# Kernel optimization log

Hardware: AMD Instinct MI355X
Metric: run time of the kernel (lower is better)

## Reference

```python
import jax, jax.numpy as jnp
import numpy as np

D_MODEL = 1024
N_HEAD = 16
HEAD_DIM = D_MODEL // N_HEAD
B, S = 4, 2048


def setup_inputs() -> dict:
    key = jax.random.key(0)
    ks = jax.random.split(key, 11)
    scale = 1.0 / np.sqrt(D_MODEL)
    inp = {
        "q": jax.random.normal(ks[0], (B, S, D_MODEL), jnp.float32),
        "k": jax.random.normal(ks[1], (B, S, D_MODEL), jnp.float32),
        "v": jax.random.normal(ks[2], (B, S, D_MODEL), jnp.float32),
        # torch nn.Linear weights: [out_features, in_features], y = x @ W.T + b
        "Wq": jax.random.normal(ks[3], (D_MODEL, D_MODEL), jnp.float32) * scale,
        "bq": jax.random.normal(ks[4], (D_MODEL,), jnp.float32) * scale,
        "Wk": jax.random.normal(ks[5], (D_MODEL, D_MODEL), jnp.float32) * scale,
        "bk": jax.random.normal(ks[6], (D_MODEL,), jnp.float32) * scale,
        "Wv": jax.random.normal(ks[7], (D_MODEL, D_MODEL), jnp.float32) * scale,
        "bv": jax.random.normal(ks[8], (D_MODEL,), jnp.float32) * scale,
        "Wo": jax.random.normal(ks[9], (D_MODEL, D_MODEL), jnp.float32) * scale,
        "bo": jax.random.normal(ks[10], (D_MODEL,), jnp.float32) * scale,
    }
    return inp


def _split_heads(x):
    # [B, S, D] -> [B, H, S, hd]
    b, s, _ = x.shape
    return x.reshape(b, s, N_HEAD, HEAD_DIM).transpose(0, 2, 1, 3)


def reference(q, k, v, Wq, bq, Wk, bk, Wv, bv, Wo, bo):
    qh = _split_heads(q @ Wq.T + bq)
    kh = _split_heads(k @ Wk.T + bk)
    vh = _split_heads(v @ Wv.T + bv)
    scores = jnp.einsum("bhqd,bhkd->bhqk", qh, kh) / jnp.sqrt(
        jnp.asarray(HEAD_DIM, qh.dtype)
    )
    weights = jax.nn.softmax(scores, axis=-1)  # [B, H, Sq, Sk]
    ctx = jnp.einsum("bhqk,bhkd->bhqd", weights, vh)
    b, h, s, d = ctx.shape
    ctx = ctx.transpose(0, 2, 1, 3).reshape(b, s, h * d)  # [B, S, D]
    return ctx @ Wo.T + bo
```

## Files before the change

### kernel.cpp

```cpp
#include <hip/hip_runtime.h>
#include <hip/hip_bf16.h>

typedef float   f32x4   __attribute__((ext_vector_type(4)));
typedef __bf16  bf16x8  __attribute__((ext_vector_type(8)));
typedef unsigned short u16x8 __attribute__((ext_vector_type(8)));
typedef unsigned short u16x4 __attribute__((ext_vector_type(4)));

#define DEVI __device__ __forceinline__

DEVI unsigned short f2bf_bits(float f) {
    __bf16 h = (__bf16)f;
    return __builtin_bit_cast(unsigned short, h);
}

DEVI f32x4 mfma_bf16(bf16x8 a, bf16x8 b, f32x4 c) {
    return __builtin_amdgcn_mfma_f32_16x16x32_bf16(a, b, c, 0, 0, 0);
}

template <bool A_F32, bool OUT_F32>
__global__ __launch_bounds__(256) void gemm_bt_kernel(
    const void* __restrict__ Ap, const float* __restrict__ W,
    const float* __restrict__ bias, void* __restrict__ Cp,
    int M, int N, int K, float scale)
{
    __shared__ __align__(16) char ldsA[128 * 128];
    __shared__ __align__(16) char ldsB[128 * 128];
    const int t = threadIdx.x;
    const int wave = t >> 6, lane = t & 63;
    const int g = lane >> 4, c = lane & 15;
    const int rowbase = blockIdx.x * 128;
    const int colbase = blockIdx.y * 128;
    const int wr = (wave >> 1) * 64, wc = (wave & 1) * 64;

    f32x4 acc[4][4] = {};

    for (int kt = 0; kt < K; kt += 64) {
#pragma unroll
        for (int ch = 0; ch < 4; ++ch) {
            int id = ch * 256 + t;
            int row = id >> 3;
            int col = (id & 7) * 8;
            int dst = row * 128 + ((col * 2) ^ ((row & 7) << 4));
            u16x8 hv;
            if constexpr (A_F32) {
                const float* src = (const float*)Ap + (size_t)(rowbase + row) * K + kt + col;
                f32x4 x0 = *(const f32x4*)src;
                f32x4 x1 = *(const f32x4*)(src + 4);
#pragma unroll
                for (int j = 0; j < 4; ++j) { hv[j] = f2bf_bits(x0[j]); hv[4 + j] = f2bf_bits(x1[j]); }
            } else {
                const unsigned short* src = (const unsigned short*)Ap + (size_t)(rowbase + row) * K + kt + col;
                hv = *(const u16x8*)src;
            }
            *(u16x8*)(ldsA + dst) = hv;

            const float* srcb = W + (size_t)(colbase + row) * K + kt + col;
            f32x4 y0 = *(const f32x4*)srcb;
            f32x4 y1 = *(const f32x4*)(srcb + 4);
            u16x8 hb;
#pragma unroll
            for (int j = 0; j < 4; ++j) { hb[j] = f2bf_bits(y0[j]); hb[4 + j] = f2bf_bits(y1[j]); }
            *(u16x8*)(ldsB + dst) = hb;
        }
        __syncthreads();

#pragma unroll
        for (int kk = 0; kk < 2; ++kk) {
            bf16x8 af[4], bfr[4];
#pragma unroll
            for (int i = 0; i < 4; ++i) {
                int ra = wr + i * 16 + c;
                af[i] = *(const bf16x8*)(ldsA + ra * 128 + ((kk * 64 + g * 16) ^ ((ra & 7) << 4)));
                int rb = wc + i * 16 + c;
                bfr[i] = *(const bf16x8*)(ldsB + rb * 128 + ((kk * 64 + g * 16) ^ ((rb & 7) << 4)));
            }
#pragma unroll
            for (int i = 0; i < 4; ++i)
#pragma unroll
                for (int j = 0; j < 4; ++j)
                    acc[i][j] = mfma_bf16(af[i], bfr[j], acc[i][j]);
        }
        __syncthreads();
    }

#pragma unroll
    for (int j = 0; j < 4; ++j) {
        int coln = colbase + wc + j * 16 + c;
        float bv = bias[coln];
#pragma unroll
        for (int i = 0; i < 4; ++i) {
            int row0 = rowbase + wr + i * 16 + g * 4;
#pragma unroll
            for (int r = 0; r < 4; ++r) {
                float val = (acc[i][j][r] + bv) * scale;
                if constexpr (OUT_F32)
                    ((float*)Cp)[(size_t)(row0 + r) * N + coln] = val;
                else
                    ((unsigned short*)Cp)[(size_t)(row0 + r) * N + coln] = f2bf_bits(val);
            }
        }
    }
}

__global__ __launch_bounds__(256) void transpose_v_kernel(
    const unsigned short* __restrict__ Vp, unsigned short* __restrict__ Vt)
{
    __shared__ unsigned short tile[64][72];
    const int t = threadIdx.x;
    const int bh = blockIdx.y, b = bh >> 4, h = bh & 15;
    const int s0 = blockIdx.x * 64;
#pragma unroll
    for (int ch = 0; ch < 2; ++ch) {
        int id = ch * 256 + t;
        int srow = id >> 3, dcol = (id & 7) * 8;
        u16x8 v = *(const u16x8*)(Vp + (size_t)(b * 2048 + s0 + srow) * 1024 + h * 64 + dcol);
        *(u16x8*)&tile[srow][dcol] = v;
    }
    __syncthreads();
#pragma unroll
    for (int ch = 0; ch < 2; ++ch) {
        int id = ch * 256 + t;
        int drow = id >> 3, scol = (id & 7) * 8;
        u16x8 ov;
#pragma unroll
        for (int j = 0; j < 8; ++j) ov[j] = tile[scol + j][drow];
        *(u16x8*)(Vt + (size_t)(bh * 64 + drow) * 2048 + s0 + scol) = ov;
    }
}

__global__ __launch_bounds__(256) void attn_kernel(
    const unsigned short* __restrict__ Qp, const unsigned short* __restrict__ Kp,
    const unsigned short* __restrict__ Vt, unsigned short* __restrict__ ctx)
{
    __shared__ __align__(16) char ldsK[64 * 128];
    __shared__ __align__(16) char ldsV[64 * 128];
    __shared__ __align__(16) char ldsP[4][16 * 128];
    const int t = threadIdx.x;
    const int wave = t >> 6, lane = t & 63;
    const int g = lane >> 4, c = lane & 15;
    const int bh = blockIdx.y, b = bh >> 4, h = bh & 15;
    const int qb = blockIdx.x * 64;

    bf16x8 qf[2];
    {
        const unsigned short* qrow = Qp + (size_t)(b * 2048 + qb + wave * 16 + c) * 1024 + h * 64;
        qf[0] = *(const bf16x8*)(qrow + 8 * g);
        qf[1] = *(const bf16x8*)(qrow + 32 + 8 * g);
    }

    f32x4 o[4] = {};
    float psum = 0.f;

    const int row0 = t >> 3, colB = (t & 7) * 8;
    const int row1 = 32 + row0;
    const int dst0 = row0 * 128 + ((colB * 2) ^ ((row0 & 7) << 4));
    const int dst1 = row1 * 128 + ((colB * 2) ^ ((row1 & 7) << 4));
    const unsigned short* Ksrc = Kp + (size_t)(b * 2048) * 1024 + h * 64;
    const unsigned short* Vsrc = Vt + (size_t)(bh * 64) * 2048;

    u16x8 kv0 = *(const u16x8*)(Ksrc + (size_t)row0 * 1024 + colB);
    u16x8 kv1 = *(const u16x8*)(Ksrc + (size_t)row1 * 1024 + colB);
    u16x8 vv0 = *(const u16x8*)(Vsrc + (size_t)row0 * 2048 + colB);
    u16x8 vv1 = *(const u16x8*)(Vsrc + (size_t)row1 * 2048 + colB);

    char* pw = ldsP[wave];

    for (int kb = 0; kb < 2048; kb += 64) {
        *(u16x8*)(ldsK + dst0) = kv0;
        *(u16x8*)(ldsK + dst1) = kv1;
        *(u16x8*)(ldsV + dst0) = vv0;
        *(u16x8*)(ldsV + dst1) = vv1;
        __syncthreads();

        if (kb + 64 < 2048) {
            kv0 = *(const u16x8*)(Ksrc + (size_t)(kb + 64 + row0) * 1024 + colB);
            kv1 = *(const u16x8*)(Ksrc + (size_t)(kb + 64 + row1) * 1024 + colB);
            vv0 = *(const u16x8*)(Vsrc + (size_t)row0 * 2048 + kb + 64 + colB);
            vv1 = *(const u16x8*)(Vsrc + (size_t)row1 * 2048 + kb + 64 + colB);
        }

        f32x4 s[4] = {};
#pragma unroll
        for (int kk = 0; kk < 2; ++kk)
#pragma unroll
            for (int ti = 0; ti < 4; ++ti) {
                int rk = ti * 16 + c;
                bf16x8 kf = *(const bf16x8*)(ldsK + rk * 128 + ((kk * 64 + g * 16) ^ ((rk & 7) << 4)));
                s[ti] = mfma_bf16(kf, qf[kk], s[ti]);
            }

        float ps0 = 0.f, ps1 = 0.f;
#pragma unroll
        for (int ti = 0; ti < 4; ++ti) {
            float p0 = __expf(s[ti][0]);
            float p1 = __expf(s[ti][1]);
            float p2 = __expf(s[ti][2]);
            float p3 = __expf(s[ti][3]);
            ps0 += p0 + p1;
            ps1 += p2 + p3;
            u16x4 hp;
            hp[0] = f2bf_bits(p0); hp[1] = f2bf_bits(p1);
            hp[2] = f2bf_bits(p2); hp[3] = f2bf_bits(p3);
            *(u16x4*)(pw + c * 128 + ((ti * 32 + g * 8) ^ ((c & 7) << 4))) = hp;
        }
        psum += ps0 + ps1;

#pragma unroll
        for (int kk = 0; kk < 2; ++kk) {
            bf16x8 pa = *(const bf16x8*)(pw + c * 128 + ((kk * 64 + g * 16) ^ ((c & 7) << 4)));
#pragma unroll
            for (int ti = 0; ti < 4; ++ti) {
                int rv = ti * 16 + c;
                bf16x8 vf = *(const bf16x8*)(ldsV + rv * 128 + ((kk * 64 + g * 16) ^ ((rv & 7) << 4)));
                o[ti] = mfma_bf16(pa, vf, o[ti]);
            }
        }
        __syncthreads();
    }

    psum += __shfl_xor(psum, 16);
    psum += __shfl_xor(psum, 32);

#pragma unroll
    for (int r = 0; r < 4; ++r) {
        float inv = 1.0f / __shfl(psum, 4 * g + r);
        int row = qb + wave * 16 + 4 * g + r;
#pragma unroll
        for (int ti = 0; ti < 4; ++ti) {
            int col = h * 64 + ti * 16 + c;
            ctx[(size_t)(b * 2048 + row) * 1024 + col] = f2bf_bits(o[ti][r] * inv);
        }
    }
}

extern "C" void kernel_launch(void* const* d_in, const int* in_sizes, int n_in,
                              void* d_out, int out_size, void* d_ws, size_t ws_size,
                              hipStream_t stream)
{
    const float* q  = (const float*)d_in[0];
    const float* k  = (const float*)d_in[1];
    const float* v  = (const float*)d_in[2];
    const float* Wq = (const float*)d_in[3];
    const float* bq = (const float*)d_in[4];
    const float* Wk = (const float*)d_in[5];
    const float* bk = (const float*)d_in[6];
    const float* Wv = (const float*)d_in[7];
    const float* bv = (const float*)d_in[8];
    const float* Wo = (const float*)d_in[9];
    const float* bo = (const float*)d_in[10];
    float* out = (float*)d_out;

    char* ws = (char*)d_ws;
    const size_t SZ = (size_t)8192 * 1024 * 2;
    unsigned short* Qp = (unsigned short*)(ws);
    unsigned short* Kp = (unsigned short*)(ws + SZ);
    unsigned short* Vp = (unsigned short*)(ws + 2 * SZ);
    unsigned short* Vt = (unsigned short*)(ws + 3 * SZ);
    unsigned short* ctx = Vp;

    dim3 gg(64, 8);
    gemm_bt_kernel<true, false><<<gg, 256, 0, stream>>>(q, Wq, bq, Qp, 8192, 1024, 1024, 0.125f);
    gemm_bt_kernel<true, false><<<gg, 256, 0, stream>>>(k, Wk, bk, Kp, 8192, 1024, 1024, 1.0f);
    gemm_bt_kernel<true, false><<<gg, 256, 0, stream>>>(v, Wv, bv, Vp, 8192, 1024, 1024, 1.0f);
    transpose_v_kernel<<<dim3(32, 64), 256, 0, stream>>>(Vp, Vt);
    attn_kernel<<<dim3(32, 64), 256, 0, stream>>>(Qp, Kp, Vt, ctx);
    gemm_bt_kernel<false, true><<<gg, 256, 0, stream>>>(ctx, Wo, bo, out, 8192, 1024, 1024, 1.0f);
}
```

Measured before the change: 254.0 us.

## Process two 16-row query tiles per wave in attention kernel

Each wave now handles 32 query rows instead of 16, so a block covers 128 queries. Each K/V fragment loaded from LDS is reused for two MFMAs, and the global K/V tile loads per query are halved. Grid size is halved accordingly. This raises register use and doubles the per-wave P scratch in LDS, which may lower occupancy.

```diff
diff --git a/kernel.cpp b/kernel.cpp
--- a/kernel.cpp
+++ b/kernel.cpp
@@ -134,22 +134,25 @@
 {
     __shared__ __align__(16) char ldsK[64 * 128];
     __shared__ __align__(16) char ldsV[64 * 128];
-    __shared__ __align__(16) char ldsP[4][16 * 128];
+    __shared__ __align__(16) char ldsP[4][2][16 * 128];
     const int t = threadIdx.x;
     const int wave = t >> 6, lane = t & 63;
     const int g = lane >> 4, c = lane & 15;
     const int bh = blockIdx.y, b = bh >> 4, h = bh & 15;
-    const int qb = blockIdx.x * 64;
-
-    bf16x8 qf[2];
+    const int qb = blockIdx.x * 128;
+
+    bf16x8 qf0[2], qf1[2];
     {
-        const unsigned short* qrow = Qp + (size_t)(b * 2048 + qb + wave * 16 + c) * 1024 + h * 64;
-        qf[0] = *(const bf16x8*)(qrow + 8 * g);
-        qf[1] = *(const bf16x8*)(qrow + 32 + 8 * g);
-    }
-
-    f32x4 o[4] = {};
-    float psum = 0.f;
+        const unsigned short* q0 = Qp + (size_t)(b * 2048 + qb + wave * 32 + c) * 1024 + h * 64;
+        qf0[0] = *(const bf16x8*)(q0 + 8 * g);
+        qf0[1] = *(const bf16x8*)(q0 + 32 + 8 * g);
+        const unsigned short* q1 = q0 + (size_t)16 * 1024;
+        qf1[0] = *(const bf16x8*)(q1 + 8 * g);
+        qf1[1] = *(const bf16x8*)(q1 + 32 + 8 * g);
+    }
+
+    f32x4 o0[4] = {}, o1[4] = {};
+    float psum0 = 0.f, psum1 = 0.f;
 
     const int row0 = t >> 3, colB = (t & 7) * 8;
     const int row1 = 32 + row0;
@@ -163,7 +166,8 @@
     u16x8 vv0 = *(const u16x8*)(Vsrc + (size_t)row0 * 2048 + colB);
     u16x8 vv1 = *(const u16x8*)(Vsrc + (size_t)row1 * 2048 + colB);
 
-    char* pw = ldsP[wave];
+    char* pw0 = ldsP[wave][0];
+    char* pw1 = ldsP[wave][1];
 
     for (int kb = 0; kb < 2048; kb += 64) {
         *(u16x8*)(ldsK + dst0) = kv0;
@@ -179,56 +183,82 @@
             vv1 = *(const u16x8*)(Vsrc + (size_t)row1 * 2048 + kb + 64 + colB);
         }
 
-        f32x4 s[4] = {};
-#pragma unroll
-        for (int kk = 0; kk < 2; ++kk)
+        f32x4 s0[4] = {}, s1[4] = {};
+#pragma unroll
+        for (int kk = 0; kk < 2; ++kk) {
+            bf16x8 kf[4];
 #pragma unroll
             for (int ti = 0; ti < 4; ++ti) {
                 int rk = ti * 16 + c;
-                bf16x8 kf = *(const bf16x8*)(ldsK + rk * 128 + ((kk * 64 + g * 16) ^ ((rk & 7) << 4)));
-                s[ti] = mfma_bf16(kf, qf[kk], s[ti]);
-            }
-
-        float ps0 = 0.f, ps1 = 0.f;
+                kf[ti] = *(const bf16x8*)(ldsK + rk * 128 + ((kk * 64 + g * 16) ^ ((rk & 7) << 4)));
+            }
+#pragma unroll
+            for (int ti = 0; ti < 4; ++ti) {
+                s0[ti] = mfma_bf16(kf[ti], qf0[kk], s0[ti]);
+                s1[ti] = mfma_bf16(kf[ti], qf1[kk], s1[ti]);
+            }
+        }
+
 #pragma unroll
         for (int ti = 0; ti < 4; ++ti) {
-            float p0 = __expf(s[ti][0]);
-            float p1 = __expf(s[ti][1]);
-            float p2 = __expf(s[ti][2]);
-            float p3 = __expf(s[ti][3]);
-            ps0 += p0 + p1;
-            ps1 += p2 + p3;
+            float p0 = __expf(s0[ti][0]);
+            float p1 = __expf(s0[ti][1]);
+            float p2 = __expf(s0[ti][2]);
+            float p3 = __expf(s0[ti][3]);
+            psum0 += (p0 + p1) + (p2 + p3);
             u16x4 hp;
             hp[0] = f2bf_bits(p0); hp[1] = f2bf_bits(p1);
             hp[2] = f2bf_bits(p2); hp[3] = f2bf_bits(p3);
-            *(u16x4*)(pw + c * 128 + ((ti * 32 + g * 8) ^ ((c & 7) << 4))) = hp;
-        }
-        psum += ps0 + ps1;
+            *(u16x4*)(pw0 + c * 128 + ((ti * 32 + g * 8) ^ ((c & 7) << 4))) = hp;
+        }
+#pragma unroll
+        for (int ti = 0; ti < 4; ++ti) {
+            float p0 = __expf(s1[ti][0]);
+            float p1 = __expf(s1[ti][1]);
+            float p2 = __expf(s1[ti][2]);
+            float p3 = __expf(s1[ti][3]);
+            psum1 += (p0 + p1) + (p2 + p3);
+            u16x4 hp;
+            hp[0] = f2bf_bits(p0); hp[1] = f2bf_bits(p1);
+            hp[2] = f2bf_bits(p2); hp[3] = f2bf_bits(p3);
+            *(u16x4*)(pw1 + c * 128 + ((ti * 32 + g * 8) ^ ((c & 7) << 4))) = hp;
+        }
 
 #pragma unroll
         for (int kk = 0; kk < 2; ++kk) {
-            bf16x8 pa = *(const bf16x8*)(pw + c * 128 + ((kk * 64 + g * 16) ^ ((c & 7) << 4)));
+            bf16x8 vf[4];
 #pragma unroll
             for (int ti = 0; ti < 4; ++ti) {
                 int rv = ti * 16 + c;
-                bf16x8 vf = *(const bf16x8*)(ldsV + rv * 128 + ((kk * 64 + g * 16) ^ ((rv & 7) << 4)));
-                o[ti] = mfma_bf16(pa, vf, o[ti]);
-            }
-        }
-        __syncthreads();
-    }
-
-    psum += __shfl_xor(psum, 16);
-    psum += __shfl_xor(psum, 32);
+                vf[ti] = *(const bf16x8*)(ldsV + rv * 128 + ((kk * 64 + g * 16) ^ ((rv & 7) << 4)));
+            }
+            bf16x8 pa0 = *(const bf16x8*)(pw0 + c * 128 + ((kk * 64 + g * 16) ^ ((c & 7) << 4)));
+            bf16x8 pa1 = *(const bf16x8*)(pw1 + c * 128 + ((kk * 64 + g * 16) ^ ((c & 7) << 4)));
+#pragma unroll
+            for (int ti = 0; ti < 4; ++ti) {
+                o0[ti] = mfma_bf16(pa0, vf[ti], o0[ti]);
+                o1[ti] = mfma_bf16(pa1, vf[ti], o1[ti]);
+            }
+        }
+        __syncthreads();
+    }
+
+    psum0 += __shfl_xor(psum0, 16);
+    psum0 += __shfl_xor(psum0, 32);
+    psum1 += __shfl_xor(psum1, 16);
+    psum1 += __shfl_xor(psum1, 32);
 
 #pragma unroll
     for (int r = 0; r < 4; ++r) {
-        float inv = 1.0f / __shfl(psum, 4 * g + r);
-        int row = qb + wave * 16 + 4 * g + r;
+        float inv0 = 1.0f / __shfl(psum0, 4 * g + r);
+        float inv1 = 1.0f / __shfl(psum1, 4 * g + r);
+        int row0q = qb + wave * 32 + 4 * g + r;
+        int row1q = row0q + 16;
 #pragma unroll
         for (int ti = 0; ti < 4; ++ti) {
             int col = h * 64 + ti * 16 + c;
-            ctx[(size_t)(b * 2048 + row) * 1024 + col] = f2bf_bits(o[ti][r] * inv);
+            ctx[(size_t)(b * 2048 + row0q) * 1024 + col] = f2bf_bits(o0[ti][r] * inv0);
+            ctx[(size_t)(b * 2048 + row1q) * 1024 + col] = f2bf_bits(o1[ti][r] * inv1);
         }
     }
 }
@@ -263,6 +293,6 @@
     gemm_bt_kernel<true, false><<<gg, 256, 0, stream>>>(k, Wk, bk, Kp, 8192, 1024, 1024, 1.0f);
     gemm_bt_kernel<true, false><<<gg, 256, 0, stream>>>(v, Wv, bv, Vp, 8192, 1024, 1024, 1.0f);
     transpose_v_kernel<<<dim3(32, 64), 256, 0, stream>>>(Vp, Vt);
-    attn_kernel<<<dim3(32, 64), 256, 0, stream>>>(Qp, Kp, Vt, ctx);
+    attn_kernel<<<dim3(16, 64), 256, 0, stream>>>(Qp, Kp, Vt, ctx);
     gemm_bt_kernel<false, true><<<gg, 256, 0, stream>>>(ctx, Wo, bo, out, 8192, 1024, 1024, 1.0f);
 }
```

Result: faster. 244.0 us (-4.0%).
